# Optimization experiments

Hardware: AMD Instinct MI355X
Metric: run time of the kernel (lower is better)

Reference implementation:

```python
import jax, jax.numpy as jnp
import numpy as np

B, NA, NB, D, NH, APO = 32, 128, 128, 512, 16, 128
VA, VB, SUP_BDIST = 64, 32, 8
INV_SQRT_2PI_FACT = (2.0 * np.pi) ** 0.5


def setup_inputs() -> dict:
    key = jax.random.key(0)
    ks = jax.random.split(key, 20)
    atoms = jax.random.randint(ks[0], (B, NA), 0, VA)
    chirals = jax.random.randint(ks[1], (B, NA), 0, 4)
    coordinates = jax.random.normal(ks[2], (B, NA, 3), dtype=jnp.float32) * 5.0
    bonds = jax.random.randint(ks[3], (B, NA, NA), 0, VB)
    i0 = jax.random.randint(ks[4], (B, NB), 0, NA)
    off = jax.random.randint(ks[5], (B, NB), 1, NA)
    i1 = (i0 + off) % NA  # guarantee distinct endpoints so one-hot sum <= 1
    bond_indices = jnp.stack([i0, i1], axis=-1)
    bond_values = jax.random.randint(ks[6], (B, NB), 0, VB)
    bdist = jax.random.randint(ks[7], (B, NA, NA), 0, SUP_BDIST)
    sc = 0.02
    # embedding tables; rows for padding_idx=0 zeroed like torch nn.Embedding
    atype_emb = (jax.random.normal(ks[8], (VA, D)) * sc).at[0].set(0.0)
    chiral_emb = (jax.random.normal(ks[9], (4, D)) * sc).at[0].set(0.0)
    apair_w_tab = jax.random.normal(ks[10], (VA * VA, APO)) * sc
    apair_b_tab = jax.random.normal(ks[11], (VA * VA, APO)) * sc
    means = jax.random.normal(ks[12], (APO,)) * 0.1
    stds = jnp.ones((APO,), jnp.float32) + jax.random.normal(ks[13], (APO,)) * 0.1
    bond_emb_tab = (jax.random.normal(ks[14], (VB, NH)) * sc).at[0].set(0.0)
    lin_W = jax.random.normal(ks[15], (APO, NH)) * (1.0 / np.sqrt(APO))
    lin_b = jax.random.normal(ks[16], (NH,)) * sc
    btype_tab = (jax.random.normal(ks[17], (VB, D)) * sc).at[0].set(0.0)
    bond_atom_tab = (jax.random.normal(ks[18], (VA, D)) * sc).at[0].set(0.0)
    ab_connect_tab = (jax.random.normal(ks[19], (2, NH)) * sc).at[0].set(0.0)
    return dict(atoms=atoms, chirals=chirals, coordinates=coordinates, bonds=bonds,
                bond_indices=bond_indices, bond_values=bond_values, bdist=bdist,
                atype_emb=atype_emb, chiral_emb=chiral_emb, apair_w_tab=apair_w_tab,
                apair_b_tab=apair_b_tab, means=means, stds=stds, bond_emb_tab=bond_emb_tab,
                lin_W=lin_W, lin_b=lin_b, btype_tab=btype_tab, bond_atom_tab=bond_atom_tab,
                ab_connect_tab=ab_connect_tab)


def reference(atoms, chirals, coordinates, bonds, bond_indices, bond_values, bdist,
              atype_emb, chiral_emb, apair_w_tab, apair_b_tab, means, stds,
              bond_emb_tab, lin_W, lin_b, btype_tab, bond_atom_tab, ab_connect_tab):
    batch, n_atom = atoms.shape
    n_bond = bond_values.shape[1]
    # --- node embeddings ---
    atoms_e = atype_emb[atoms] + chiral_emb[chirals]                 # [B,Na,D]
    bonds_e = btype_tab[bond_values]                                  # [B,Nb,D]
    a0 = jnp.take_along_axis(atoms, bond_indices[:, :, 0], axis=1)    # [B,Nb]
    a1 = jnp.take_along_axis(atoms, bond_indices[:, :, 1], axis=1)
    bonds_e = bonds_e + bond_atom_tab[a0] + bond_atom_tab[a1]
    atoms_emb = jnp.concatenate([atoms_e, bonds_e], axis=1).transpose(1, 0, 2)  # [Na+Nb,B,D]
    # --- pairwise distances + RBF-modulated pair features ---
    diff = coordinates[:, None, :, :] - coordinates[:, :, None, :]    # [B,Na,Na,3]
    distances = jnp.sqrt(jnp.sum(diff * diff, axis=-1))               # [B,Na,Na]
    pair_idx = atoms[:, None, :] * VA + atoms[:, :, None]             # [B,Na,Na]
    x = apair_w_tab[pair_idx] * distances[..., None] + apair_b_tab[pair_idx]  # [B,Na,Na,APO]
    s = jnp.abs(stds) + 1e-5
    x = jnp.exp(-0.5 * jnp.square((x - means) / s)) / (INV_SQRT_2PI_FACT * s)
    apairs = jnp.einsum('bijp,ph->bijh', x, lin_W) + lin_b + bond_emb_tab[bonds]  # [B,Na,Na,NH]
    # --- atom-bond connectivity block ---
    oh = (jax.nn.one_hot(bond_indices[:, :, 0], n_atom, dtype=jnp.int32)
          + jax.nn.one_hot(bond_indices[:, :, 1], n_atom, dtype=jnp.int32))      # [B,Nb,Na]
    oh = oh * (bond_values != 0).astype(jnp.int32)[..., None]
    abpairs = ab_connect_tab[oh]                                       # [B,Nb,Na,NH]
    top = jnp.concatenate([apairs, abpairs], axis=1)                   # [B,Na+Nb,Na,NH]
    right = jnp.concatenate([abpairs.transpose(0, 2, 1, 3),
                             jnp.zeros((batch, n_bond, n_bond, NH), apairs.dtype)], axis=1)
    apairs = jnp.concatenate([top, right], axis=2)                     # [B,L,L,NH]
    padding_mask = jnp.concatenate([atoms == 0, bond_values == 0], axis=1)  # [B,L]
    apairs = jnp.where(padding_mask[:, None, :, None], -jnp.inf, apairs)
    apairs = apairs.transpose(0, 3, 1, 2)                              # [B,NH,L,L]
    # --- extended bdist ---
    oh_d = oh * SUP_BDIST
    bdist_out = jnp.concatenate([
        jnp.concatenate([bdist, oh_d], axis=1),
        jnp.concatenate([oh_d.transpose(0, 2, 1),
                         jnp.zeros((batch, n_bond, n_bond), oh_d.dtype)], axis=1)], axis=2)
    return atoms_emb, apairs, bdist_out, padding_mask
```

## Files before the change

kernel.cpp:

```cpp
#include <hip/hip_runtime.h>
#include <hip/hip_fp16.h>
#include <math.h>

#define B_ 32
#define NA_ 128
#define NB_ 128
#define D_ 512
#define NH_ 16
#define APO_ 128
#define L_ 256
#define VA_ 64

#define NEG_BIG (-3.0e38f)

#define WSB_WBT  2048
#define WSB_WBF  8192
#define WSB_BBF  (8192 + (1 << 20))
#define WS_NEED_BYTES (8192 + (2 << 20))

typedef __attribute__((ext_vector_type(8))) _Float16 f16x8;
typedef __attribute__((ext_vector_type(4))) float f32x4;

#define TROW 136

__global__ __launch_bounds__(256) void k0_fold(
    const float* __restrict__ wtab, const float* __restrict__ btab,
    const float* __restrict__ means, const float* __restrict__ stds,
    const float* __restrict__ linW, char* __restrict__ wsb) {
    int t = blockIdx.x * 256 + threadIdx.x;
    int ai = t >> 13;
    int aj = (t >> 7) & 63;
    int p = t & (APO_ - 1);
    int src = (aj << 13) + (ai << 7) + p;
    float s = fabsf(stds[p]) + 1e-5f;
    float si = 1.0f / s;
    _Float16* wbf = (_Float16*)(wsb + WSB_WBF);
    _Float16* bbf = (_Float16*)(wsb + WSB_BBF);
    wbf[t] = (_Float16)(wtab[src] * si);
    bbf[t] = (_Float16)((btab[src] - means[p]) * si);
    if (blockIdx.x == 0) {
        _Float16* wbT = (_Float16*)(wsb + WSB_WBT);
        for (int q = threadIdx.x; q < NH_ * APO_; q += 256) {
            int h = q >> 7, pp = q & 127;
            float s2 = fabsf(stds[pp]) + 1e-5f;
            float cof = 0.39894228040143270f / s2;
            wbT[q] = (_Float16)(linW[pp * NH_ + h] * cof);
        }
    }
}

__global__ __launch_bounds__(256, 4) void k2_mfma(
    const int* __restrict__ atoms, const float* __restrict__ coords,
    const int* __restrict__ bonds, const float* __restrict__ linb,
    const float* __restrict__ bond_emb, const char* __restrict__ wsb,
    float* __restrict__ out1) {
    __shared__ _Float16 tab[2][64 * TROW];
    float (*epi)[129] = (float (*)[129]) & tab[0][0];

    int b = blockIdx.x >> 7;
    int i = blockIdx.x & (NA_ - 1);
    int tid = threadIdx.x;
    int wave = tid >> 6;
    int lane = tid & 63;
    int col = lane & 15;
    int kg = lane >> 4;

    int ai = atoms[b * NA_ + i];

    const _Float16* gw = (const _Float16*)(wsb + WSB_WBF) + (size_t)ai * (64 * APO_);
    const _Float16* gb = (const _Float16*)(wsb + WSB_BBF) + (size_t)ai * (64 * APO_);
#pragma unroll
    for (int it = 0; it < 4; ++it) {
        int g = (it * 256 + tid) * 8;
        int row = g >> 7, off = g & 127;
        *(f16x8*)&tab[0][row * TROW + off] = *(const f16x8*)(gw + g);
        *(f16x8*)&tab[1][row * TROW + off] = *(const f16x8*)(gb + g);
    }

    int j2 = tid & 127;
    int hg = tid >> 7;
    int ajr2 = atoms[b * NA_ + j2];
    int bij2 = bonds[((size_t)b * NA_ + i) * NA_ + j2];
    const float4* ber4 = (const float4*)(bond_emb + (size_t)bij2 * NH_);
    float4 berA = ber4[hg * 2 + 0];
    float4 berB = ber4[hg * 2 + 1];

    float cx = coords[((size_t)b * NA_ + i) * 3 + 0];
    float cy = coords[((size_t)b * NA_ + i) * 3 + 1];
    float cz = coords[((size_t)b * NA_ + i) * 3 + 2];
    __half2 d2[2];
    int rowh[2];
#pragma unroll
    for (int tt = 0; tt < 2; ++tt) {
        int jA = (wave * 2 + tt) * 16 + col;
        int ajt = atoms[b * NA_ + jA];
        float dx = coords[((size_t)b * NA_ + jA) * 3 + 0] - cx;
        float dy = coords[((size_t)b * NA_ + jA) * 3 + 1] - cy;
        float dz = coords[((size_t)b * NA_ + jA) * 3 + 2] - cz;
        float dist = sqrtf(dx * dx + dy * dy + dz * dz);
        d2[tt] = __float2half2_rn(dist);
        rowh[tt] = ajt * TROW;
    }

    const _Float16* wbT = (const _Float16*)(wsb + WSB_WBT);
    f16x8 Bf[4];
#pragma unroll
    for (int ks = 0; ks < 4; ++ks)
        Bf[ks] = *(const f16x8*)(wbT + col * APO_ + ks * 32 + kg * 8);

    const __half2 KE2 = __float2half2_rn(-0.72134752044448170f);

    __syncthreads();

    f32x4 accv[2];
#pragma unroll
    for (int tt = 0; tt < 2; ++tt) {
        f32x4 acc = {0.f, 0.f, 0.f, 0.f};
#pragma unroll
        for (int ks = 0; ks < 4; ++ks) {
            f16x8 w8 = *(const f16x8*)&tab[0][rowh[tt] + ks * 32 + kg * 8];
            f16x8 b8 = *(const f16x8*)&tab[1][rowh[tt] + ks * 32 + kg * 8];
            const __half2* wh = (const __half2*)&w8;
            const __half2* bh = (const __half2*)&b8;
            f16x8 af;
            __half2* eh = (__half2*)&af;
#pragma unroll
            for (int q = 0; q < 4; ++q) {
                __half2 xh = __hfma2(wh[q], d2[tt], bh[q]);
                __half2 t2 = __hmul2(__hmul2(xh, xh), KE2);
                eh[q] = h2exp2(t2);
            }
            acc = __builtin_amdgcn_mfma_f32_16x16x32_f16(af, Bf[ks], acc, 0, 0, 0);
        }
        accv[tt] = acc;
    }
    __syncthreads();

#pragma unroll
    for (int tt = 0; tt < 2; ++tt) {
        int jb = (wave * 2 + tt) * 16;
#pragma unroll
        for (int r = 0; r < 4; ++r)
            epi[col][jb + kg * 4 + r] = accv[tt][r];
    }
    __syncthreads();

    float berx[8] = {berA.x, berA.y, berA.z, berA.w, berB.x, berB.y, berB.z, berB.w};
    bool maskj = (ajr2 == 0);
    float* opb = out1 + (size_t)b * NH_ * L_ * L_ + (size_t)(hg * 8) * (L_ * L_)
               + (size_t)i * L_ + j2;
#pragma unroll
    for (int q = 0; q < 8; ++q) {
        int h = hg * 8 + q;
        float v = epi[h][j2] + linb[h] + berx[q];
        opb[(size_t)q * (L_ * L_)] = maskj ? NEG_BIG : v;
    }
}

__global__ __launch_bounds__(128) void k2_pair(
    const int* __restrict__ atoms, const float* __restrict__ coords,
    const int* __restrict__ bonds, const float* __restrict__ wtab,
    const float* __restrict__ btab, const float* __restrict__ linW,
    const float* __restrict__ linb, const float* __restrict__ bond_emb,
    const float* __restrict__ means, const float* __restrict__ stds,
    float* __restrict__ out1) {
    int b = blockIdx.x >> 7;
    int i = blockIdx.x & (NA_ - 1);
    int j = threadIdx.x;
    int ai = atoms[b * NA_ + i];
    int aj = atoms[b * NA_ + j];
    float cx = coords[((size_t)b * NA_ + i) * 3 + 0];
    float cy = coords[((size_t)b * NA_ + i) * 3 + 1];
    float cz = coords[((size_t)b * NA_ + i) * 3 + 2];
    float dx = coords[((size_t)b * NA_ + j) * 3 + 0] - cx;
    float dy = coords[((size_t)b * NA_ + j) * 3 + 1] - cy;
    float dz = coords[((size_t)b * NA_ + j) * 3 + 2] - cz;
    float dist = sqrtf(dx * dx + dy * dy + dz * dz);
    int idx = aj * VA_ + ai;
    const float4* wrow = (const float4*)(wtab + (size_t)idx * APO_);
    const float4* brow = (const float4*)(btab + (size_t)idx * APO_);
    float acc[NH_];
#pragma unroll
    for (int h = 0; h < NH_; ++h) acc[h] = 0.0f;
    const float KE = -0.72134752044448170f;
    for (int pp = 0; pp < APO_ / 4; ++pp) {
        float4 w4 = wrow[pp];
        float4 b4 = brow[pp];
        const float* wq = (const float*)&w4;
        const float* bq = (const float*)&b4;
#pragma unroll
        for (int q = 0; q < 4; ++q) {
            int p = pp * 4 + q;
            float s = fabsf(stds[p]) + 1e-5f;
            float si = 1.0f / s;
            float xh = fmaf(wq[q] * si, dist, fmaf(bq[q], si, -means[p] * si));
            float g = si * 0.39894228040143270f * exp2f(KE * xh * xh);
            const float* Wr = linW + p * NH_;
#pragma unroll
            for (int h = 0; h < NH_; ++h) acc[h] = fmaf(g, Wr[h], acc[h]);
        }
    }
    int bij = bonds[((size_t)b * NA_ + i) * NA_ + j];
    bool maskj = (aj == 0);
    float* op = out1 + (size_t)b * NH_ * L_ * L_ + (size_t)i * L_ + j;
#pragma unroll
    for (int h = 0; h < NH_; ++h) {
        float v = acc[h] + linb[h] + bond_emb[(size_t)bij * NH_ + h];
        op[(size_t)h * (L_ * L_)] = maskj ? NEG_BIG : v;
    }
}

__global__ __launch_bounds__(256) void k_fill(
    const int* __restrict__ atoms, const int* __restrict__ chirals,
    const int* __restrict__ bond_idx, const int* __restrict__ bond_vals,
    const int* __restrict__ bdist,
    const float* __restrict__ atype, const float* __restrict__ chiral_t,
    const float* __restrict__ btype, const float* __restrict__ batom,
    const float* __restrict__ ab_tab,
    float* __restrict__ out0, float* __restrict__ out1,
    float* __restrict__ out2, float* __restrict__ out3) {
    int b = blockIdx.x >> 8;
    int r = blockIdx.x & 255;
    int c = threadIdx.x;

    {
        float2 v;
        if (r < NA_) {
            int a = atoms[b * NA_ + r];
            int ch = chirals[b * NA_ + r];
            float2 v1 = ((const float2*)(atype + (size_t)a * D_))[c];
            float2 v2 = ((const float2*)(chiral_t + (size_t)ch * D_))[c];
            v = make_float2(v1.x + v2.x, v1.y + v2.y);
        } else {
            int k = r - NA_;
            int bv = bond_vals[b * NB_ + k];
            int i0 = bond_idx[(b * NB_ + k) * 2 + 0];
            int i1 = bond_idx[(b * NB_ + k) * 2 + 1];
            int a0 = atoms[b * NA_ + i0];
            int a1 = atoms[b * NA_ + i1];
            float2 v1 = ((const float2*)(btype + (size_t)bv * D_))[c];
            float2 v2 = ((const float2*)(batom + (size_t)a0 * D_))[c];
            float2 v3 = ((const float2*)(batom + (size_t)a1 * D_))[c];
            v = make_float2(v1.x + v2.x + v3.x, v1.y + v2.y + v3.y);
        }
        ((float2*)(out0 + ((size_t)r * B_ + b) * D_))[c] = v;
    }

    {
        float v = 0.0f;
        if (r < NA_) {
            if (c < NA_) {
                v = (float)bdist[((size_t)b * NA_ + r) * NA_ + c];
            } else {
                int k = c - NA_;
                int bv = bond_vals[b * NB_ + k];
                int i0 = bond_idx[(b * NB_ + k) * 2 + 0];
                int i1 = bond_idx[(b * NB_ + k) * 2 + 1];
                v = (bv != 0 && (i0 == r || i1 == r)) ? 8.0f : 0.0f;
            }
        } else if (c < NA_) {
            int k = r - NA_;
            int bv = bond_vals[b * NB_ + k];
            int i0 = bond_idx[(b * NB_ + k) * 2 + 0];
            int i1 = bond_idx[(b * NB_ + k) * 2 + 1];
            v = (bv != 0 && (i0 == c || i1 == c)) ? 8.0f : 0.0f;
        }
        out2[((size_t)b * L_ + r) * L_ + c] = v;
    }

    if (r == 0) {
        bool m = (c < NA_) ? (atoms[b * NA_ + c] == 0)
                           : (bond_vals[b * NB_ + (c - NA_)] == 0);
        out3[b * L_ + c] = m ? 1.0f : 0.0f;
    }

    if (r >= NA_ || c >= NA_) {
        float ohv = 0.0f;
        bool mask;
        if (c < NA_) {
            int k = r - NA_;
            int bv = bond_vals[b * NB_ + k];
            int i0 = bond_idx[(b * NB_ + k) * 2 + 0];
            int i1 = bond_idx[(b * NB_ + k) * 2 + 1];
            ohv = (bv != 0 && (i0 == c || i1 == c)) ? 1.0f : 0.0f;
            mask = (atoms[b * NA_ + c] == 0);
        } else {
            int k = c - NA_;
            int bv = bond_vals[b * NB_ + k];
            mask = (bv == 0);
            if (r < NA_) {
                int i0 = bond_idx[(b * NB_ + k) * 2 + 0];
                int i1 = bond_idx[(b * NB_ + k) * 2 + 1];
                ohv = (bv != 0 && (i0 == r || i1 == r)) ? 1.0f : 0.0f;
            }
        }
        float* op = out1 + (size_t)b * NH_ * L_ * L_ + (size_t)r * L_ + c;
#pragma unroll
        for (int h = 0; h < NH_; ++h) {
            float v = mask ? NEG_BIG : ohv * ab_tab[NH_ + h];
            op[(size_t)h * (L_ * L_)] = v;
        }
    }
}

extern "C" void kernel_launch(void* const* d_in, const int* in_sizes, int n_in,
                              void* d_out, int out_size, void* d_ws, size_t ws_size,
                              hipStream_t stream) {
    const int*   atoms     = (const int*)d_in[0];
    const int*   chirals   = (const int*)d_in[1];
    const float* coords    = (const float*)d_in[2];
    const int*   bonds     = (const int*)d_in[3];
    const int*   bond_idx  = (const int*)d_in[4];
    const int*   bond_vals = (const int*)d_in[5];
    const int*   bdist     = (const int*)d_in[6];
    const float* atype     = (const float*)d_in[7];
    const float* chiral_t  = (const float*)d_in[8];
    const float* wtab      = (const float*)d_in[9];
    const float* btab      = (const float*)d_in[10];
    const float* means     = (const float*)d_in[11];
    const float* stds      = (const float*)d_in[12];
    const float* bond_emb  = (const float*)d_in[13];
    const float* linW      = (const float*)d_in[14];
    const float* linb      = (const float*)d_in[15];
    const float* btype     = (const float*)d_in[16];
    const float* batom     = (const float*)d_in[17];
    const float* ab_tab    = (const float*)d_in[18];

    float* out  = (float*)d_out;
    float* out0 = out;
    float* out1 = out0 + (size_t)L_ * B_ * D_;
    float* out2 = out1 + (size_t)B_ * NH_ * L_ * L_;
    float* out3 = out2 + (size_t)B_ * L_ * L_;
    char*  wsb  = (char*)d_ws;

    bool use_fold = ws_size >= (size_t)WS_NEED_BYTES;

    if (use_fold) {
        hipLaunchKernelGGL(k0_fold, dim3(VA_ * VA_ * APO_ / 256), dim3(256), 0, stream,
                           wtab, btab, means, stds, linW, wsb);
        hipLaunchKernelGGL(k2_mfma, dim3(B_ * NA_), dim3(256), 0, stream,
                           atoms, coords, bonds, linb, bond_emb, wsb, out1);
    } else {
        hipLaunchKernelGGL(k2_pair, dim3(B_ * NA_), dim3(NA_), 0, stream,
                           atoms, coords, bonds, wtab, btab, linW, linb, bond_emb,
                           means, stds, out1);
    }
    hipLaunchKernelGGL(k_fill, dim3(B_ * L_), dim3(256), 0, stream,
                       atoms, chirals, bond_idx, bond_vals, bdist,
                       atype, chiral_t, btype, batom, ab_tab,
                       out0, out1, out2, out3);
}
```

Baseline: 52.99 us.

## Fuse pair-MFMA and fill kernels into one heterogeneous launch with vectorized stores

Merges the MFMA pair kernel and the fill kernel into one launch: the first B*NA blocks compute the atom-pair bias and the extra blocks write embeddings, bdist, bond-region bias and the mask. This drops one kernel launch and its serialization gap, and lets the memory-bound fill work overlap with the compute blocks. The fill work now uses float4 loads and stores with four rows per block, and the pair epilogue writes float4 rows (epilogue LDS stride changed to 132). The cost is extra register pressure and divergent block roles inside one kernel, which could lower occupancy.

```diff
diff --git a/kernel.cpp b/kernel.cpp
--- a/kernel.cpp
+++ b/kernel.cpp
@@ -22,6 +22,7 @@
 typedef __attribute__((ext_vector_type(4))) float f32x4;
 
 #define TROW 136
+#define EPIW 132
 
 __global__ __launch_bounds__(256) void k0_fold(
     const float* __restrict__ wtab, const float* __restrict__ btab,
@@ -49,111 +50,234 @@
     }
 }
 
-__global__ __launch_bounds__(256, 4) void k2_mfma(
-    const int* __restrict__ atoms, const float* __restrict__ coords,
-    const int* __restrict__ bonds, const float* __restrict__ linb,
+__global__ __launch_bounds__(256, 4) void k_mega(
+    const int* __restrict__ atoms, const int* __restrict__ chirals,
+    const float* __restrict__ coords, const int* __restrict__ bonds,
+    const int* __restrict__ bond_idx, const int* __restrict__ bond_vals,
+    const int* __restrict__ bdist,
+    const float* __restrict__ atype, const float* __restrict__ chiral_t,
+    const float* __restrict__ btype, const float* __restrict__ batom,
+    const float* __restrict__ ab_tab, const float* __restrict__ linb,
     const float* __restrict__ bond_emb, const char* __restrict__ wsb,
-    float* __restrict__ out1) {
+    float* __restrict__ out0, float* __restrict__ out1,
+    float* __restrict__ out2, float* __restrict__ out3) {
     __shared__ _Float16 tab[2][64 * TROW];
-    float (*epi)[129] = (float (*)[129]) & tab[0][0];
-
-    int b = blockIdx.x >> 7;
-    int i = blockIdx.x & (NA_ - 1);
+    float (*epi)[EPIW] = (float (*)[EPIW]) & tab[0][0];
+
     int tid = threadIdx.x;
-    int wave = tid >> 6;
-    int lane = tid & 63;
-    int col = lane & 15;
-    int kg = lane >> 4;
-
-    int ai = atoms[b * NA_ + i];
-
-    const _Float16* gw = (const _Float16*)(wsb + WSB_WBF) + (size_t)ai * (64 * APO_);
-    const _Float16* gb = (const _Float16*)(wsb + WSB_BBF) + (size_t)ai * (64 * APO_);
-#pragma unroll
-    for (int it = 0; it < 4; ++it) {
-        int g = (it * 256 + tid) * 8;
-        int row = g >> 7, off = g & 127;
-        *(f16x8*)&tab[0][row * TROW + off] = *(const f16x8*)(gw + g);
-        *(f16x8*)&tab[1][row * TROW + off] = *(const f16x8*)(gb + g);
-    }
-
-    int j2 = tid & 127;
-    int hg = tid >> 7;
-    int ajr2 = atoms[b * NA_ + j2];
-    int bij2 = bonds[((size_t)b * NA_ + i) * NA_ + j2];
-    const float4* ber4 = (const float4*)(bond_emb + (size_t)bij2 * NH_);
-    float4 berA = ber4[hg * 2 + 0];
-    float4 berB = ber4[hg * 2 + 1];
-
-    float cx = coords[((size_t)b * NA_ + i) * 3 + 0];
-    float cy = coords[((size_t)b * NA_ + i) * 3 + 1];
-    float cz = coords[((size_t)b * NA_ + i) * 3 + 2];
-    __half2 d2[2];
-    int rowh[2];
-#pragma unroll
-    for (int tt = 0; tt < 2; ++tt) {
-        int jA = (wave * 2 + tt) * 16 + col;
-        int ajt = atoms[b * NA_ + jA];
-        float dx = coords[((size_t)b * NA_ + jA) * 3 + 0] - cx;
-        float dy = coords[((size_t)b * NA_ + jA) * 3 + 1] - cy;
-        float dz = coords[((size_t)b * NA_ + jA) * 3 + 2] - cz;
-        float dist = sqrtf(dx * dx + dy * dy + dz * dz);
-        d2[tt] = __float2half2_rn(dist);
-        rowh[tt] = ajt * TROW;
-    }
-
-    const _Float16* wbT = (const _Float16*)(wsb + WSB_WBT);
-    f16x8 Bf[4];
-#pragma unroll
-    for (int ks = 0; ks < 4; ++ks)
-        Bf[ks] = *(const f16x8*)(wbT + col * APO_ + ks * 32 + kg * 8);
-
-    const __half2 KE2 = __float2half2_rn(-0.72134752044448170f);
-
-    __syncthreads();
-
-    f32x4 accv[2];
-#pragma unroll
-    for (int tt = 0; tt < 2; ++tt) {
-        f32x4 acc = {0.f, 0.f, 0.f, 0.f};
-#pragma unroll
-        for (int ks = 0; ks < 4; ++ks) {
-            f16x8 w8 = *(const f16x8*)&tab[0][rowh[tt] + ks * 32 + kg * 8];
-            f16x8 b8 = *(const f16x8*)&tab[1][rowh[tt] + ks * 32 + kg * 8];
-            const __half2* wh = (const __half2*)&w8;
-            const __half2* bh = (const __half2*)&b8;
-            f16x8 af;
-            __half2* eh = (__half2*)&af;
-#pragma unroll
-            for (int q = 0; q < 4; ++q) {
-                __half2 xh = __hfma2(wh[q], d2[tt], bh[q]);
-                __half2 t2 = __hmul2(__hmul2(xh, xh), KE2);
-                eh[q] = h2exp2(t2);
-            }
-            acc = __builtin_amdgcn_mfma_f32_16x16x32_f16(af, Bf[ks], acc, 0, 0, 0);
-        }
-        accv[tt] = acc;
-    }
-    __syncthreads();
-
-#pragma unroll
-    for (int tt = 0; tt < 2; ++tt) {
-        int jb = (wave * 2 + tt) * 16;
-#pragma unroll
-        for (int r = 0; r < 4; ++r)
-            epi[col][jb + kg * 4 + r] = accv[tt][r];
-    }
-    __syncthreads();
-
-    float berx[8] = {berA.x, berA.y, berA.z, berA.w, berB.x, berB.y, berB.z, berB.w};
-    bool maskj = (ajr2 == 0);
-    float* opb = out1 + (size_t)b * NH_ * L_ * L_ + (size_t)(hg * 8) * (L_ * L_)
-               + (size_t)i * L_ + j2;
-#pragma unroll
-    for (int q = 0; q < 8; ++q) {
-        int h = hg * 8 + q;
-        float v = epi[h][j2] + linb[h] + berx[q];
-        opb[(size_t)q * (L_ * L_)] = maskj ? NEG_BIG : v;
+
+    if (blockIdx.x < B_ * NA_) {
+        int b = blockIdx.x >> 7;
+        int i = blockIdx.x & (NA_ - 1);
+        int wave = tid >> 6;
+        int lane = tid & 63;
+        int col = lane & 15;
+        int kg = lane >> 4;
+
+        int ai = atoms[b * NA_ + i];
+
+        const _Float16* gw = (const _Float16*)(wsb + WSB_WBF) + (size_t)ai * (64 * APO_);
+        const _Float16* gb = (const _Float16*)(wsb + WSB_BBF) + (size_t)ai * (64 * APO_);
+#pragma unroll
+        for (int it = 0; it < 4; ++it) {
+            int g = (it * 256 + tid) * 8;
+            int row = g >> 7, off = g & 127;
+            *(f16x8*)&tab[0][row * TROW + off] = *(const f16x8*)(gw + g);
+            *(f16x8*)&tab[1][row * TROW + off] = *(const f16x8*)(gb + g);
+        }
+
+        float cx = coords[((size_t)b * NA_ + i) * 3 + 0];
+        float cy = coords[((size_t)b * NA_ + i) * 3 + 1];
+        float cz = coords[((size_t)b * NA_ + i) * 3 + 2];
+        __half2 d2[2];
+        int rowh[2];
+#pragma unroll
+        for (int tt = 0; tt < 2; ++tt) {
+            int jA = (wave * 2 + tt) * 16 + col;
+            int ajt = atoms[b * NA_ + jA];
+            float dx = coords[((size_t)b * NA_ + jA) * 3 + 0] - cx;
+            float dy = coords[((size_t)b * NA_ + jA) * 3 + 1] - cy;
+            float dz = coords[((size_t)b * NA_ + jA) * 3 + 2] - cz;
+            float dist = sqrtf(dx * dx + dy * dy + dz * dz);
+            d2[tt] = __float2half2_rn(dist);
+            rowh[tt] = ajt * TROW;
+        }
+
+        const _Float16* wbT = (const _Float16*)(wsb + WSB_WBT);
+        f16x8 Bf[4];
+#pragma unroll
+        for (int ks = 0; ks < 4; ++ks)
+            Bf[ks] = *(const f16x8*)(wbT + col * APO_ + ks * 32 + kg * 8);
+
+        const __half2 KE2 = __float2half2_rn(-0.72134752044448170f);
+
+        __syncthreads();
+
+        f32x4 accv[2];
+#pragma unroll
+        for (int tt = 0; tt < 2; ++tt) {
+            f32x4 acc = {0.f, 0.f, 0.f, 0.f};
+#pragma unroll
+            for (int ks = 0; ks < 4; ++ks) {
+                f16x8 w8 = *(const f16x8*)&tab[0][rowh[tt] + ks * 32 + kg * 8];
+                f16x8 b8 = *(const f16x8*)&tab[1][rowh[tt] + ks * 32 + kg * 8];
+                const __half2* wh = (const __half2*)&w8;
+                const __half2* bh = (const __half2*)&b8;
+                f16x8 af;
+                __half2* eh = (__half2*)&af;
+#pragma unroll
+                for (int q = 0; q < 4; ++q) {
+                    __half2 xh = __hfma2(wh[q], d2[tt], bh[q]);
+                    __half2 t2 = __hmul2(__hmul2(xh, xh), KE2);
+                    eh[q] = h2exp2(t2);
+                }
+                acc = __builtin_amdgcn_mfma_f32_16x16x32_f16(af, Bf[ks], acc, 0, 0, 0);
+            }
+            accv[tt] = acc;
+        }
+        __syncthreads();
+
+#pragma unroll
+        for (int tt = 0; tt < 2; ++tt) {
+            int jb = (wave * 2 + tt) * 16;
+#pragma unroll
+            for (int rr = 0; rr < 4; ++rr)
+                epi[col][jb + kg * 4 + rr] = accv[tt][rr];
+        }
+        __syncthreads();
+
+        int h2 = tid >> 5;
+        int c0 = (tid & 31) << 2;
+        int4 aj4 = *(const int4*)(atoms + b * NA_ + c0);
+        int4 bj4 = *(const int4*)(bonds + ((size_t)b * NA_ + i) * NA_ + c0);
+        float* opb = out1 + (size_t)b * NH_ * L_ * L_ + (size_t)i * L_;
+#pragma unroll
+        for (int hi = 0; hi < 2; ++hi) {
+            int h = h2 + hi * 8;
+            float lb = linb[h];
+            float4 vv = *(const float4*)&epi[h][c0];
+            vv.x += lb + bond_emb[(size_t)bj4.x * NH_ + h];
+            vv.y += lb + bond_emb[(size_t)bj4.y * NH_ + h];
+            vv.z += lb + bond_emb[(size_t)bj4.z * NH_ + h];
+            vv.w += lb + bond_emb[(size_t)bj4.w * NH_ + h];
+            if (aj4.x == 0) vv.x = NEG_BIG;
+            if (aj4.y == 0) vv.y = NEG_BIG;
+            if (aj4.z == 0) vv.z = NEG_BIG;
+            if (aj4.w == 0) vv.w = NEG_BIG;
+            *(float4*)(opb + (size_t)h * (L_ * L_) + c0) = vv;
+        }
+    } else {
+        int idx = blockIdx.x - B_ * NA_;
+        int b = idx >> 6;
+        int g = idx & 63;
+        int rloc = tid >> 6;
+        int t64 = tid & 63;
+        int r = g * 4 + rloc;
+
+        if (r < NA_) {
+            int a = atoms[b * NA_ + r];
+            int ch = chirals[b * NA_ + r];
+            const float4* A = (const float4*)(atype + (size_t)a * D_);
+            const float4* C = (const float4*)(chiral_t + (size_t)ch * D_);
+            float4* O = (float4*)(out0 + ((size_t)r * B_ + b) * D_);
+#pragma unroll
+            for (int it = 0; it < 2; ++it) {
+                int c4 = t64 + 64 * it;
+                float4 v1 = A[c4], v2 = C[c4];
+                O[c4] = make_float4(v1.x + v2.x, v1.y + v2.y, v1.z + v2.z, v1.w + v2.w);
+            }
+        } else {
+            int k = r - NA_;
+            int bv = bond_vals[b * NB_ + k];
+            int i0 = bond_idx[(b * NB_ + k) * 2 + 0];
+            int i1 = bond_idx[(b * NB_ + k) * 2 + 1];
+            int a0 = atoms[b * NA_ + i0];
+            int a1 = atoms[b * NA_ + i1];
+            const float4* T = (const float4*)(btype + (size_t)bv * D_);
+            const float4* P = (const float4*)(batom + (size_t)a0 * D_);
+            const float4* Q = (const float4*)(batom + (size_t)a1 * D_);
+            float4* O = (float4*)(out0 + ((size_t)r * B_ + b) * D_);
+#pragma unroll
+            for (int it = 0; it < 2; ++it) {
+                int c4 = t64 + 64 * it;
+                float4 v1 = T[c4], v2 = P[c4], v3 = Q[c4];
+                O[c4] = make_float4(v1.x + v2.x + v3.x, v1.y + v2.y + v3.y,
+                                    v1.z + v2.z + v3.z, v1.w + v2.w + v3.w);
+            }
+        }
+
+        int c0 = t64 << 2;
+        float ab1[NH_];
+#pragma unroll
+        for (int h = 0; h < NH_; ++h) ab1[h] = ab_tab[NH_ + h];
+
+        if (r < NA_) {
+            float4 v2v;
+            if (c0 < NA_) {
+                int4 d4 = *(const int4*)(bdist + ((size_t)b * NA_ + r) * NA_ + c0);
+                v2v = make_float4((float)d4.x, (float)d4.y, (float)d4.z, (float)d4.w);
+                *(float4*)(out2 + ((size_t)b * L_ + r) * L_ + c0) = v2v;
+            } else {
+                int k0 = c0 - NA_;
+                int4 bv4 = *(const int4*)(bond_vals + b * NB_ + k0);
+                int4 p01 = *(const int4*)(bond_idx + (b * NB_ + k0) * 2);
+                int4 p23 = *(const int4*)(bond_idx + (b * NB_ + k0) * 2 + 4);
+                float o0 = (bv4.x && (p01.x == r || p01.y == r)) ? 1.0f : 0.0f;
+                float o1 = (bv4.y && (p01.z == r || p01.w == r)) ? 1.0f : 0.0f;
+                float o2 = (bv4.z && (p23.x == r || p23.y == r)) ? 1.0f : 0.0f;
+                float o3 = (bv4.w && (p23.z == r || p23.w == r)) ? 1.0f : 0.0f;
+                *(float4*)(out2 + ((size_t)b * L_ + r) * L_ + c0) =
+                    make_float4(o0 * 8.f, o1 * 8.f, o2 * 8.f, o3 * 8.f);
+                float* op = out1 + (size_t)b * NH_ * L_ * L_ + (size_t)r * L_ + c0;
+#pragma unroll
+                for (int h = 0; h < NH_; ++h) {
+                    float4 vv;
+                    vv.x = bv4.x ? o0 * ab1[h] : NEG_BIG;
+                    vv.y = bv4.y ? o1 * ab1[h] : NEG_BIG;
+                    vv.z = bv4.z ? o2 * ab1[h] : NEG_BIG;
+                    vv.w = bv4.w ? o3 * ab1[h] : NEG_BIG;
+                    *(float4*)(op + (size_t)h * (L_ * L_)) = vv;
+                }
+            }
+        } else {
+            int k = r - NA_;
+            int bvr = bond_vals[b * NB_ + k];
+            int i0r = bond_idx[(b * NB_ + k) * 2 + 0];
+            int i1r = bond_idx[(b * NB_ + k) * 2 + 1];
+            float o0 = 0.f, o1 = 0.f, o2 = 0.f, o3 = 0.f;
+            bool m0, m1, m2, m3;
+            if (c0 < NA_) {
+                o0 = (bvr && (i0r == c0 + 0 || i1r == c0 + 0)) ? 1.0f : 0.0f;
+                o1 = (bvr && (i0r == c0 + 1 || i1r == c0 + 1)) ? 1.0f : 0.0f;
+                o2 = (bvr && (i0r == c0 + 2 || i1r == c0 + 2)) ? 1.0f : 0.0f;
+                o3 = (bvr && (i0r == c0 + 3 || i1r == c0 + 3)) ? 1.0f : 0.0f;
+                int4 aj4 = *(const int4*)(atoms + b * NA_ + c0);
+                m0 = (aj4.x == 0); m1 = (aj4.y == 0); m2 = (aj4.z == 0); m3 = (aj4.w == 0);
+                *(float4*)(out2 + ((size_t)b * L_ + r) * L_ + c0) =
+                    make_float4(o0 * 8.f, o1 * 8.f, o2 * 8.f, o3 * 8.f);
+            } else {
+                int4 bv4 = *(const int4*)(bond_vals + b * NB_ + (c0 - NA_));
+                m0 = (bv4.x == 0); m1 = (bv4.y == 0); m2 = (bv4.z == 0); m3 = (bv4.w == 0);
+                *(float4*)(out2 + ((size_t)b * L_ + r) * L_ + c0) =
+                    make_float4(0.f, 0.f, 0.f, 0.f);
+            }
+            float* op = out1 + (size_t)b * NH_ * L_ * L_ + (size_t)r * L_ + c0;
+#pragma unroll
+            for (int h = 0; h < NH_; ++h) {
+                float4 vv;
+                vv.x = m0 ? NEG_BIG : o0 * ab1[h];
+                vv.y = m1 ? NEG_BIG : o1 * ab1[h];
+                vv.z = m2 ? NEG_BIG : o2 * ab1[h];
+                vv.w = m3 ? NEG_BIG : o3 * ab1[h];
+                *(float4*)(op + (size_t)h * (L_ * L_)) = vv;
+            }
+        }
+
+        if (g == 0) {
+            bool m = (tid < NA_) ? (atoms[b * NA_ + tid] == 0)
+                                 : (bond_vals[b * NB_ + (tid - NA_)] == 0);
+            out3[b * L_ + tid] = m ? 1.0f : 0.0f;
+        }
     }
 }
 
@@ -222,7 +346,6 @@
     int b = blockIdx.x >> 8;
     int r = blockIdx.x & 255;
     int c = threadIdx.x;
-
     {
         float2 v;
         if (r < NA_) {
@@ -245,7 +368,6 @@
         }
         ((float2*)(out0 + ((size_t)r * B_ + b) * D_))[c] = v;
     }
-
     {
         float v = 0.0f;
         if (r < NA_) {
@@ -267,13 +389,11 @@
         }
         out2[((size_t)b * L_ + r) * L_ + c] = v;
     }
-
     if (r == 0) {
         bool m = (c < NA_) ? (atoms[b * NA_ + c] == 0)
                            : (bond_vals[b * NB_ + (c - NA_)] == 0);
         out3[b * L_ + c] = m ? 1.0f : 0.0f;
     }
-
     if (r >= NA_ || c >= NA_) {
         float ohv = 0.0f;
         bool mask;
@@ -338,15 +458,17 @@
     if (use_fold) {
         hipLaunchKernelGGL(k0_fold, dim3(VA_ * VA_ * APO_ / 256), dim3(256), 0, stream,
                            wtab, btab, means, stds, linW, wsb);
-        hipLaunchKernelGGL(k2_mfma, dim3(B_ * NA_), dim3(256), 0, stream,
-                           atoms, coords, bonds, linb, bond_emb, wsb, out1);
+        hipLaunchKernelGGL(k_mega, dim3(B_ * NA_ + B_ * 64), dim3(256), 0, stream,
+                           atoms, chirals, coords, bonds, bond_idx, bond_vals, bdist,
+                           atype, chiral_t, btype, batom, ab_tab, linb, bond_emb, wsb,
+                           out0, out1, out2, out3);
     } else {
         hipLaunchKernelGGL(k2_pair, dim3(B_ * NA_), dim3(NA_), 0, stream,
                            atoms, coords, bonds, wtab, btab, linW, linb, bond_emb,
                            means, stds, out1);
-    }
-    hipLaunchKernelGGL(k_fill, dim3(B_ * L_), dim3(256), 0, stream,
-                       atoms, chirals, bond_idx, bond_vals, bdist,
-                       atype, chiral_t, btype, batom, ab_tab,
-                       out0, out1, out2, out3);
+        hipLaunchKernelGGL(k_fill, dim3(B_ * L_), dim3(256), 0, stream,
+                           atoms, chirals, bond_idx, bond_vals, bdist,
+                           atype, chiral_t, btype, batom, ab_tab,
+                           out0, out1, out2, out3);
+    }
 }
```

After: 54.27 us. +2.4%, slower.
